# Kernel tuning notes

Hardware: AMD Instinct MI355X
Metric: run time of the kernel (lower is better)

The kernel has to match this reference:

```python
import jax, jax.numpy as jnp
import numpy as np

N_PER_GRAPH = 468
B = 32
N = B * N_PER_GRAPH            # 14976 nodes
E = 89600                      # synthetic Delaunay-like directed edges
IN_DIM, HID, OUT, HEADS = 2, 256, 512, 4
NEG_SLOPE = 0.2
EPS = 1e-16


def setup_inputs() -> dict:
    key = jax.random.key(0)
    ks = jax.random.split(key, 12)
    x = jax.random.uniform(ks[0], (N, IN_DIM), dtype=jnp.float32)
    edge_index = jax.random.randint(ks[1], (2, E), 0, N, dtype=jnp.int64)
    batch = jnp.repeat(jnp.arange(B, dtype=jnp.int64), N_PER_GRAPH)
    s1 = 1.0 / np.sqrt(IN_DIM)
    s2 = 1.0 / np.sqrt(HID)
    sg = 1.0 / np.sqrt(OUT)
    return {
        "x": x,
        "edge_index": edge_index,
        "batch": batch,
        # GATConv 1: in_dim -> hidden, heads=4, concat=False
        "W1": jax.random.normal(ks[2], (IN_DIM, HEADS * HID), jnp.float32) * s1,
        "a1_src": jax.random.normal(ks[3], (HEADS, HID), jnp.float32) * s2,
        "a1_dst": jax.random.normal(ks[4], (HEADS, HID), jnp.float32) * s2,
        "b1": jnp.zeros((HID,), jnp.float32),
        # GATConv 2: hidden -> out, heads=4, concat=False
        "W2": jax.random.normal(ks[5], (HID, HEADS * OUT), jnp.float32) * s2,
        "a2_src": jax.random.normal(ks[6], (HEADS, OUT), jnp.float32) * sg,
        "a2_dst": jax.random.normal(ks[7], (HEADS, OUT), jnp.float32) * sg,
        "b2": jnp.zeros((OUT,), jnp.float32),
        # GlobalAttention gate_nn: Linear(out_dim, 1)
        "Wg": jax.random.normal(ks[8], (OUT, 1), jnp.float32) * sg,
        "bg": jnp.zeros((1,), jnp.float32),
    }


def _gat_layer(x, src, dst, W, a_src, a_dst, b, heads, out_ch):
    n = x.shape[0]
    xh = (x @ W).reshape(n, heads, out_ch)            # [N,H,C]
    alpha_s = jnp.einsum("nhc,hc->nh", xh, a_src)     # [N,H]
    alpha_d = jnp.einsum("nhc,hc->nh", xh, a_dst)
    e = alpha_s[src] + alpha_d[dst]                   # [E,H]
    e = jnp.where(e > 0, e, NEG_SLOPE * e)            # leaky_relu(0.2)
    # segment softmax over incoming edges of each destination node
    m = jax.ops.segment_max(e, dst, num_segments=n)
    ex = jnp.exp(e - m[dst])
    denom = jax.ops.segment_sum(ex, dst, num_segments=n)
    alpha = ex / (denom[dst] + EPS)                   # [E,H]
    msg = xh[src] * alpha[:, :, None]                 # [E,H,C]
    out = jax.ops.segment_sum(msg, dst, num_segments=n)  # [N,H,C]
    return out.mean(axis=1) + b                       # concat=False -> head mean


def reference(x, edge_index, batch, W1, a1_src, a1_dst, b1,
              W2, a2_src, a2_dst, b2, Wg, bg):
    n = x.shape[0]
    # PyG GATConv default add_self_loops=True (both layers use the same graph)
    loops = jnp.arange(n, dtype=edge_index.dtype)
    src = jnp.concatenate([edge_index[0], loops])
    dst = jnp.concatenate([edge_index[1], loops])

    h = _gat_layer(x, src, dst, W1, a1_src, a1_dst, b1, HEADS, HID)
    h = jax.nn.relu(h)
    h = _gat_layer(h, src, dst, W2, a2_src, a2_dst, b2, HEADS, OUT)
    h = jax.nn.relu(h)

    # GlobalAttention pooling: gate = Linear(out,1), softmax per graph, weighted sum
    gate = h @ Wg + bg                                # [N,1]
    gm = jax.ops.segment_max(gate, batch, num_segments=B)
    ge = jnp.exp(gate - gm[batch])
    gs = jax.ops.segment_sum(ge, batch, num_segments=B)
    attn = ge / (gs[batch] + EPS)                     # [N,1]
    pooled = jax.ops.segment_sum(attn * h, batch, num_segments=B)  # [B,512]
    return pooled.reshape(-1, 1, OUT)                 # [B,1,512]
```

## Files before the change

### kernel.cpp

```cpp
#include <hip/hip_runtime.h>
#include <hip/hip_bf16.h>
#include <math.h>

#define HEADS 4
#define C1 256
#define C2 512
#define NEG 0.2f
#define EPSF 1e-16f
#define DCAP 64

using bf16x8 = __attribute__((ext_vector_type(8))) short;
using f32x4  = __attribute__((ext_vector_type(4))) float;

__device__ __forceinline__ float lrelu(float e) { return e > 0.f ? e : NEG * e; }

__device__ __forceinline__ unsigned short f2bf(float v) {
    __hip_bfloat16 b = __float2bfloat16(v);
    return *reinterpret_cast<unsigned short*>(&b);
}
__device__ __forceinline__ float bf2f(unsigned short u) {
    __hip_bfloat16 b = *reinterpret_cast<__hip_bfloat16*>(&u);
    return __bfloat162float(b);
}


__global__ __launch_bounds__(256) void k1_prep(
    const float* __restrict__ x, const float* __restrict__ W1,
    const float* __restrict__ a1s, const float* __restrict__ a1d,
    const float* __restrict__ W2, const float* __restrict__ a2s, const float* __restrict__ a2d,
    const int* __restrict__ ei, int E, int N,
    float* __restrict__ as1, float* __restrict__ ad1,
    float* __restrict__ w2a,
    unsigned short* __restrict__ W2t_hi, unsigned short* __restrict__ W2t_lo,
    int* __restrict__ deg, int* __restrict__ bucket)
{
    int b = blockIdx.x, tid = threadIdx.x;
    int wv = tid >> 6, lane = tid & 63;
    if (b < 59) {
        __shared__ float s_w1a[16];
#pragma unroll
        for (int q = 0; q < 4; q++) {
            int o = wv * 4 + q, sd = o >> 3, idx = o & 7, h = idx >> 1, d = idx & 1;
            const float* av = sd ? a1d : a1s;
            float p = 0.f;
            for (int c = lane; c < 256; c += 64) p += W1[d * 1024 + h * 256 + c] * av[h * 256 + c];
#pragma unroll
            for (int m = 32; m >= 1; m >>= 1) p += __shfl_xor(p, m, 64);
            if (lane == 0) s_w1a[o] = p;
        }
        __syncthreads();
        int n = b * 256 + tid;
        if (n < N) {
            float x0 = x[2 * n], x1 = x[2 * n + 1];
            float4 av, dv;
            float* ap = &av.x; float* dp = &dv.x;
#pragma unroll
            for (int h = 0; h < 4; h++) {
                ap[h] = x0 * s_w1a[h * 2] + x1 * s_w1a[h * 2 + 1];
                dp[h] = x0 * s_w1a[8 + h * 2] + x1 * s_w1a[8 + h * 2 + 1];
            }
            *reinterpret_cast<float4*>(&as1[n * 4]) = av;
            *reinterpret_cast<float4*>(&ad1[n * 4]) = dv;
        }
    } else if (b < 67) {
        int bb = b - 59, sd = bb >> 2, h = bb & 3;
        const float* av = sd ? a2d : a2s;
        float gv[8];
#pragma unroll
        for (int q = 0; q < 8; q++) gv[q] = av[h * 512 + lane * 8 + q];
        for (int k = wv; k < 256; k += 4) {
            const float4 w0 = *reinterpret_cast<const float4*>(&W2[(size_t)k * 2048 + h * 512 + lane * 8]);
            const float4 w1 = *reinterpret_cast<const float4*>(&W2[(size_t)k * 2048 + h * 512 + lane * 8 + 4]);
            float p = w0.x*gv[0] + w0.y*gv[1] + w0.z*gv[2] + w0.w*gv[3]
                    + w1.x*gv[4] + w1.y*gv[5] + w1.z*gv[6] + w1.w*gv[7];
#pragma unroll
            for (int m = 32; m >= 1; m >>= 1) p += __shfl_xor(p, m, 64);
            if (lane == 0) w2a[sd * 1024 + h * 256 + k] = p;
        }
    } else if (b < 195) {
        __shared__ float T[64][65];
        int lin = b - 67;
        int kk0 = (lin & 15) * 64, n0 = (lin >> 4) * 64;
        int h = kk0 >> 8, k0 = kk0 & 255;
#pragma unroll
        for (int rr = 0; rr < 16; rr++) {
            int ki = rr * 4 + (tid >> 6), ni = tid & 63;
            T[ki][ni] = W2[(size_t)(k0 + ki) * 2048 + h * 512 + n0 + ni];
        }
        __syncthreads();
#pragma unroll
        for (int rr = 0; rr < 16; rr++) {
            int ni = rr * 4 + (tid >> 6), ki = tid & 63;
            float v = T[ki][ni];
            unsigned short hi = f2bf(v);
            unsigned short lo = f2bf(v - bf2f(hi));
            size_t o = (size_t)(n0 + ni) * 1024 + kk0 + ki;
            W2t_hi[o] = hi; W2t_lo[o] = lo;
        }
    } else {
        int i = (b - 195) * 256 + tid;
        if (i < E) {
            int s = ei[i], d = ei[E + i];
            int slot = atomicAdd(&deg[d], 1);
            if (slot < DCAP) bucket[d * DCAP + slot] = s;
        }
    }
}

__global__ __launch_bounds__(256) void k4_agg1_h1(
    const float* __restrict__ x, const float* __restrict__ as1, const float* __restrict__ ad1,
    const int* __restrict__ deg, const int* __restrict__ bucket,
    const float* __restrict__ W1, const float* __restrict__ b1, const float* __restrict__ w2a,
    float* __restrict__ h1, float* __restrict__ as2, float* __restrict__ ad2)
{
    int wv = threadIdx.x >> 6, lane = threadIdx.x & 63;
    int n = blockIdx.x * 4 + wv;
    const float4 sa4 = *reinterpret_cast<const float4*>(&as1[n * 4]);
    const float4 da4 = *reinterpret_cast<const float4*>(&ad1[n * 4]);
    const float sa[4] = {sa4.x, sa4.y, sa4.z, sa4.w};
    const float da[4] = {da4.x, da4.y, da4.z, da4.w};
    float acc[8] = {0,0,0,0,0,0,0,0};
    float den[4] = {0,0,0,0};
    int dg = min(deg[n], DCAP);
    for (int i = lane; i < dg; i += 64) {
        int s = bucket[n * DCAP + i];
        const float4 a4 = *reinterpret_cast<const float4*>(&as1[s * 4]);
        const float af[4] = {a4.x, a4.y, a4.z, a4.w};
        const float2 xv = reinterpret_cast<const float2*>(x)[s];
#pragma unroll
        for (int q = 0; q < 4; q++) {
            float w = expf(lrelu(af[q] + da[q]));
            den[q] += w;
            acc[2 * q]     = fmaf(w, xv.x, acc[2 * q]);
            acc[2 * q + 1] = fmaf(w, xv.y, acc[2 * q + 1]);
        }
    }
#pragma unroll
    for (int msk = 1; msk <= 32; msk <<= 1) {
#pragma unroll
        for (int q = 0; q < 8; q++) acc[q] += __shfl_xor(acc[q], msk, 64);
#pragma unroll
        for (int q = 0; q < 4; q++) den[q] += __shfl_xor(den[q], msk, 64);
    }
    const float2 xn = reinterpret_cast<const float2*>(x)[n];
    float xa[8];
#pragma unroll
    for (int q = 0; q < 4; q++) {
        float ws = expf(lrelu(sa[q] + da[q]));
        float dq = den[q] + ws;
        float inv = 1.f / (dq + EPSF);
        xa[2 * q]     = (acc[2 * q]     + ws * xn.x) * inv;
        xa[2 * q + 1] = (acc[2 * q + 1] + ws * xn.y) * inv;
    }
    float t[4] = {0.f, 0.f, 0.f, 0.f};
#pragma unroll
    for (int h = 0; h < 4; h++)
#pragma unroll
        for (int d = 0; d < 2; d++) {
            const float4 w4 = *reinterpret_cast<const float4*>(&W1[d * 1024 + h * 256 + lane * 4]);
            float xx = xa[h * 2 + d];
            t[0] = fmaf(xx, w4.x, t[0]);
            t[1] = fmaf(xx, w4.y, t[1]);
            t[2] = fmaf(xx, w4.z, t[2]);
            t[3] = fmaf(xx, w4.w, t[3]);
        }
    const float4 b4 = *reinterpret_cast<const float4*>(&b1[lane * 4]);
    float v[4];
    v[0] = fmaxf(fmaf(0.25f, t[0], b4.x), 0.f);
    v[1] = fmaxf(fmaf(0.25f, t[1], b4.y), 0.f);
    v[2] = fmaxf(fmaf(0.25f, t[2], b4.z), 0.f);
    v[3] = fmaxf(fmaf(0.25f, t[3], b4.w), 0.f);
    *reinterpret_cast<float4*>(&h1[(size_t)n * 256 + lane * 4]) = make_float4(v[0], v[1], v[2], v[3]);
    float p[8];
#pragma unroll
    for (int o = 0; o < 8; o++) {
        int sd = o >> 2, h = o & 3;
        const float4 w4 = *reinterpret_cast<const float4*>(&w2a[sd * 1024 + h * 256 + lane * 4]);
        p[o] = v[0] * w4.x + v[1] * w4.y + v[2] * w4.z + v[3] * w4.w;
    }
#pragma unroll
    for (int msk = 1; msk <= 32; msk <<= 1)
#pragma unroll
        for (int o = 0; o < 8; o++) p[o] += __shfl_xor(p[o], msk, 64);
    if (lane == 0) {
        *reinterpret_cast<float4*>(&as2[n * 4]) = make_float4(p[0], p[1], p[2], p[3]);
        *reinterpret_cast<float4*>(&ad2[n * 4]) = make_float4(p[4], p[5], p[6], p[7]);
    }
}

__global__ __launch_bounds__(256) void k6_agg2(
    const float* __restrict__ h1, const float* __restrict__ as2, const float* __restrict__ ad2,
    const int* __restrict__ deg, const int* __restrict__ bucket,
    unsigned short* __restrict__ hagg_hi, unsigned short* __restrict__ hagg_lo)
{
    int wv = threadIdx.x >> 6, lane = threadIdx.x & 63;
    int n = blockIdx.x * 4 + wv;
    const float4 sa4 = *reinterpret_cast<const float4*>(&as2[n * 4]);
    const float4 da4 = *reinterpret_cast<const float4*>(&ad2[n * 4]);
    const float sa[4] = {sa4.x, sa4.y, sa4.z, sa4.w};
    const float da[4] = {da4.x, da4.y, da4.z, da4.w};
    float den[4], acc[4][4];
    const float4 hs = *reinterpret_cast<const float4*>(&h1[(size_t)n * 256 + lane * 4]);
    const float hv0[4] = {hs.x, hs.y, hs.z, hs.w};
#pragma unroll
    for (int h = 0; h < 4; h++) {
        float ws = expf(lrelu(sa[h] + da[h]));
        den[h] = ws;
#pragma unroll
        for (int q = 0; q < 4; q++) acc[h][q] = ws * hv0[q];
    }
    int dg = min(deg[n], DCAP);
    for (int i = 0; i < dg; i++) {
        int s = bucket[n * DCAP + i];
        const float4 a4 = *reinterpret_cast<const float4*>(&as2[s * 4]);
        const float af[4] = {a4.x, a4.y, a4.z, a4.w};
        const float4 hv = *reinterpret_cast<const float4*>(&h1[(size_t)s * 256 + lane * 4]);
#pragma unroll
        for (int h = 0; h < 4; h++) {
            float w = expf(lrelu(af[h] + da[h]));
            den[h] += w;
            acc[h][0] = fmaf(w, hv.x, acc[h][0]);
            acc[h][1] = fmaf(w, hv.y, acc[h][1]);
            acc[h][2] = fmaf(w, hv.z, acc[h][2]);
            acc[h][3] = fmaf(w, hv.w, acc[h][3]);
        }
    }
#pragma unroll
    for (int h = 0; h < 4; h++) {
        float inv = 1.f / (den[h] + EPSF);
        ushort4 hi4, lo4;
        unsigned short* hp = &hi4.x; unsigned short* lp = &lo4.x;
#pragma unroll
        for (int q = 0; q < 4; q++) {
            float val = acc[h][q] * inv;
            unsigned short hi = f2bf(val);
            hp[q] = hi;
            lp[q] = f2bf(val - bf2f(hi));
        }
        size_t o = (size_t)n * 1024 + h * 256 + lane * 4;
        *reinterpret_cast<ushort4*>(&hagg_hi[o]) = hi4;
        *reinterpret_cast<ushort4*>(&hagg_lo[o]) = lo4;
    }
}

__global__ __launch_bounds__(256) void k7_gemm2(
    const unsigned short* __restrict__ Ahi, const unsigned short* __restrict__ Alo,
    const unsigned short* __restrict__ Bhi, const unsigned short* __restrict__ Blo,
    const float* __restrict__ b2, const float* __restrict__ Wg,
    float* __restrict__ h2, float* __restrict__ gate)
{
    __shared__ __align__(16) unsigned short As_hi[128 * 40], As_lo[128 * 40];
    __shared__ __align__(16) unsigned short Bs_hi[128 * 40], Bs_lo[128 * 40];
    __shared__ float s_gate[128];
    int tid = threadIdx.x, l = tid & 63, wv = tid >> 6;
    int wr = wv >> 1, wc = wv & 1;
    int bid = blockIdx.x, rtile, ctile;
    if (bid < 448) { rtile = (bid & 7) + 8 * (bid >> 5); ctile = (bid >> 3) & 3; }
    else           { int t = bid - 448; rtile = 112 + (t >> 2); ctile = t & 3; }
    int row0 = rtile * 128, col0 = ctile * 128;
    int lm = l & 15, lg = l >> 4;
    if (tid < 128) s_gate[tid] = 0.f;

    int r0 = tid >> 2, k00 = (tid & 3) * 8;
    int r1 = (tid + 256) >> 2, k01 = ((tid + 256) & 3) * 8;

    f32x4 acc[4][4];
#pragma unroll
    for (int i = 0; i < 4; i++)
#pragma unroll
        for (int jj = 0; jj < 4; jj++) { acc[i][jj][0]=0.f; acc[i][jj][1]=0.f; acc[i][jj][2]=0.f; acc[i][jj][3]=0.f; }

    uint4 pah0, pal0, pbh0, pbl0, pah1, pal1, pbh1, pbl1;
    {
        size_t ga0 = (size_t)(row0 + r0) * 1024 + k00, gb0 = (size_t)(col0 + r0) * 1024 + k00;
        size_t ga1 = (size_t)(row0 + r1) * 1024 + k01, gb1 = (size_t)(col0 + r1) * 1024 + k01;
        pah0 = *reinterpret_cast<const uint4*>(Ahi + ga0); pal0 = *reinterpret_cast<const uint4*>(Alo + ga0);
        pbh0 = *reinterpret_cast<const uint4*>(Bhi + gb0); pbl0 = *reinterpret_cast<const uint4*>(Blo + gb0);
        pah1 = *reinterpret_cast<const uint4*>(Ahi + ga1); pal1 = *reinterpret_cast<const uint4*>(Alo + ga1);
        pbh1 = *reinterpret_cast<const uint4*>(Bhi + gb1); pbl1 = *reinterpret_cast<const uint4*>(Blo + gb1);
    }

    for (int kt = 0; kt < 1024; kt += 32) {
        *reinterpret_cast<uint4*>(&As_hi[r0 * 40 + k00]) = pah0;
        *reinterpret_cast<uint4*>(&As_lo[r0 * 40 + k00]) = pal0;
        *reinterpret_cast<uint4*>(&Bs_hi[r0 * 40 + k00]) = pbh0;
        *reinterpret_cast<uint4*>(&Bs_lo[r0 * 40 + k00]) = pbl0;
        *reinterpret_cast<uint4*>(&As_hi[r1 * 40 + k01]) = pah1;
        *reinterpret_cast<uint4*>(&As_lo[r1 * 40 + k01]) = pal1;
        *reinterpret_cast<uint4*>(&Bs_hi[r1 * 40 + k01]) = pbh1;
        *reinterpret_cast<uint4*>(&Bs_lo[r1 * 40 + k01]) = pbl1;
        __syncthreads();
        if (kt + 32 < 1024) {
            int ktn = kt + 32;
            size_t ga0 = (size_t)(row0 + r0) * 1024 + ktn + k00, gb0 = (size_t)(col0 + r0) * 1024 + ktn + k00;
            size_t ga1 = (size_t)(row0 + r1) * 1024 + ktn + k01, gb1 = (size_t)(col0 + r1) * 1024 + ktn + k01;
            pah0 = *reinterpret_cast<const uint4*>(Ahi + ga0); pal0 = *reinterpret_cast<const uint4*>(Alo + ga0);
            pbh0 = *reinterpret_cast<const uint4*>(Bhi + gb0); pbl0 = *reinterpret_cast<const uint4*>(Blo + gb0);
            pah1 = *reinterpret_cast<const uint4*>(Ahi + ga1); pal1 = *reinterpret_cast<const uint4*>(Alo + ga1);
            pbh1 = *reinterpret_cast<const uint4*>(Bhi + gb1); pbl1 = *reinterpret_cast<const uint4*>(Blo + gb1);
        }
        bf16x8 ah[4], al[4], bh[4], bl[4];
#pragma unroll
        for (int i = 0; i < 4; i++) {
            int base = (wr * 64 + i * 16 + lm) * 40 + lg * 8;
            ah[i] = *reinterpret_cast<const bf16x8*>(&As_hi[base]);
            al[i] = *reinterpret_cast<const bf16x8*>(&As_lo[base]);
        }
#pragma unroll
        for (int jj = 0; jj < 4; jj++) {
            int base = (wc * 64 + jj * 16 + lm) * 40 + lg * 8;
            bh[jj] = *reinterpret_cast<const bf16x8*>(&Bs_hi[base]);
            bl[jj] = *reinterpret_cast<const bf16x8*>(&Bs_lo[base]);
        }
#pragma unroll
        for (int i = 0; i < 4; i++)
#pragma unroll
            for (int jj = 0; jj < 4; jj++) {
                acc[i][jj] = __builtin_amdgcn_mfma_f32_16x16x32_bf16(ah[i], bh[jj], acc[i][jj], 0, 0, 0);
                acc[i][jj] = __builtin_amdgcn_mfma_f32_16x16x32_bf16(ah[i], bl[jj], acc[i][jj], 0, 0, 0);
                acc[i][jj] = __builtin_amdgcn_mfma_f32_16x16x32_bf16(al[i], bh[jj], acc[i][jj], 0, 0, 0);
            }
        __syncthreads();
    }
    float b2c[4], wgj[4];
#pragma unroll
    for (int jj = 0; jj < 4; jj++) {
        int col = col0 + wc * 64 + jj * 16 + lm;
        b2c[jj] = b2[col]; wgj[jj] = Wg[col];
    }
#pragma unroll
    for (int i = 0; i < 4; i++) {
#pragma unroll
        for (int r = 0; r < 4; r++) {
            int row = row0 + wr * 64 + i * 16 + lg * 4 + r;
            float g = 0.f;
#pragma unroll
            for (int jj = 0; jj < 4; jj++) {
                float v = fmaxf(fmaf(0.25f, acc[i][jj][r], b2c[jj]), 0.f);
                h2[(size_t)row * 512 + col0 + wc * 64 + jj * 16 + lm] = v;
                g = fmaf(v, wgj[jj], g);
            }
            g += __shfl_xor(g, 1, 64);
            g += __shfl_xor(g, 2, 64);
            g += __shfl_xor(g, 4, 64);
            g += __shfl_xor(g, 8, 64);
            if (lm == 0) atomicAdd(&s_gate[wr * 64 + i * 16 + lg * 4 + r], g);
        }
    }
    __syncthreads();
    if (tid < 128) atomicAdd(&gate[row0 + tid], s_gate[tid]);
}

__global__ __launch_bounds__(256) void k8_pool(
    const float* __restrict__ gate, const float* __restrict__ h2,
    float* __restrict__ out, int npg)
{
    int bq = blockIdx.x, cs = blockIdx.y, tid = threadIdx.x;
    int n0 = bq * npg;
    __shared__ float sw[512];
    __shared__ float sred[4];
    __shared__ float4 sacc[256];
    float part = 0.f;
    for (int i = tid; i < 512; i += 256) {
        float e = (i < npg) ? expf(gate[n0 + i]) : 0.f;
        sw[i] = e; part += e;
    }
#pragma unroll
    for (int m = 32; m >= 1; m >>= 1) part += __shfl_xor(part, m, 64);
    if ((tid & 63) == 0) sred[tid >> 6] = part;
    __syncthreads();
    float inv = 1.f / (sred[0] + sred[1] + sred[2] + sred[3] + EPSF);
    int slot = tid & 31, sub = tid >> 5;
    const float* base = h2 + (size_t)n0 * 512 + cs * 128 + slot * 4;
    float4 acc = make_float4(0.f, 0.f, 0.f, 0.f);
    for (int i = sub; i < npg; i += 8) {
        float w = sw[i];
        const float4 v = *reinterpret_cast<const float4*>(base + (size_t)i * 512);
        acc.x = fmaf(w, v.x, acc.x);
        acc.y = fmaf(w, v.y, acc.y);
        acc.z = fmaf(w, v.z, acc.z);
        acc.w = fmaf(w, v.w, acc.w);
    }
    sacc[tid] = acc;
    __syncthreads();
    if (sub == 0) {
        float4 t = acc;
#pragma unroll
        for (int s2 = 1; s2 < 8; s2++) {
            const float4 o = sacc[s2 * 32 + slot];
            t.x += o.x; t.y += o.y; t.z += o.z; t.w += o.w;
        }
        t.x *= inv; t.y *= inv; t.z *= inv; t.w *= inv;
        *reinterpret_cast<float4*>(&out[(size_t)bq * 512 + cs * 128 + slot * 4]) = t;
    }
}

extern "C" void kernel_launch(void* const* d_in, const int* in_sizes, int n_in,
                              void* d_out, int out_size, void* d_ws, size_t ws_size,
                              hipStream_t stream)
{
    const float* x    = (const float*)d_in[0];
    const int*   ei   = (const int*)d_in[1];
    const float* W1   = (const float*)d_in[3];
    const float* a1s  = (const float*)d_in[4];
    const float* a1d  = (const float*)d_in[5];
    const float* b1   = (const float*)d_in[6];
    const float* W2   = (const float*)d_in[7];
    const float* a2s  = (const float*)d_in[8];
    const float* a2d  = (const float*)d_in[9];
    const float* b2   = (const float*)d_in[10];
    const float* Wg   = (const float*)d_in[11];
    float* out = (float*)d_out;

    const int N = in_sizes[0] / 2;
    const int E = in_sizes[1] / 2;
    const int Bq = out_size / C2;
    const int npg = N / Bq;

    char* w = (char*)d_ws;
    size_t off = 0;
    auto alloc = [&](size_t bytes) { void* p = w + off; off += (bytes + 255) & ~(size_t)255; return p; };

    float* h1       = (float*)alloc((size_t)N * 256 * 4);
    float* h2       = (float*)alloc((size_t)N * 512 * 4);
    unsigned short* hagg_hi = (unsigned short*)alloc((size_t)N * 1024 * 2);
    unsigned short* hagg_lo = (unsigned short*)alloc((size_t)N * 1024 * 2);
    unsigned short* W2t_hi  = (unsigned short*)alloc((size_t)512 * 1024 * 2);
    unsigned short* W2t_lo  = (unsigned short*)alloc((size_t)512 * 1024 * 2);
    float* as1   = (float*)alloc((size_t)N * 4 * 4);
    float* ad1   = (float*)alloc((size_t)N * 4 * 4);
    float* as2   = (float*)alloc((size_t)N * 4 * 4);
    float* ad2   = (float*)alloc((size_t)N * 4 * 4);
    int*   deg   = (int*)alloc((size_t)N * 4);
    float* gate  = (float*)alloc((size_t)N * 4);
    float* w2a   = (float*)alloc(2048 * 4);
    int*   bucket = (int*)alloc((size_t)N * DCAP * 4);
    (void)ws_size; (void)n_in;

    const int EB = (E + 255) / 256;

    hipMemsetAsync(deg, 0, (size_t)N * 4 * 2, stream);

    k1_prep<<<195 + EB, 256, 0, stream>>>(x, W1, a1s, a1d, W2, a2s, a2d, ei, E, N,
                                          as1, ad1, w2a, W2t_hi, W2t_lo, deg, bucket);
    k4_agg1_h1<<<N / 4, 256, 0, stream>>>(x, as1, ad1, deg, bucket,
                                          W1, b1, w2a, h1, as2, ad2);
    k6_agg2<<<N / 4, 256, 0, stream>>>(h1, as2, ad2, deg, bucket, hagg_hi, hagg_lo);
    k7_gemm2<<<468, 256, 0, stream>>>(hagg_hi, hagg_lo, W2t_hi, W2t_lo,
                                      b2, Wg, h2, gate);
    k8_pool<<<dim3(Bq, 4), 256, 0, stream>>>(gate, h2, out, npg);
}
```

Baseline: 251.4 us.

## Fuse pipeline into two persistent kernels with software grid barriers

Merges prep, layer-1 aggregation and layer-2 aggregation into one persistent kernel, and the GEMM plus pooling into a second, separated by atomic-counter grid barriers. This removes kernel launch gaps and boundaries between stages. The pooling stage is also split across more blocks. It relies on all blocks being co-resident, and the barriers add spin cost; grid-stride loops over the aggregation replace one-block-per-4-nodes launches.

```diff
diff --git a/kernel.cpp b/kernel.cpp
--- a/kernel.cpp
+++ b/kernel.cpp
@@ -23,235 +23,258 @@
     return __bfloat162float(b);
 }
 
-
-__global__ __launch_bounds__(256) void k1_prep(
+__device__ __forceinline__ void gbar(int* cnt, int* gen, int nb, int e) {
+    __syncthreads();
+    if (threadIdx.x == 0) {
+        __threadfence();
+        int v = __hip_atomic_fetch_add(cnt, 1, __ATOMIC_RELAXED, __HIP_MEMORY_SCOPE_AGENT);
+        if (v == nb * e - 1) {
+            __hip_atomic_fetch_add(gen, 1, __ATOMIC_RELEASE, __HIP_MEMORY_SCOPE_AGENT);
+        } else {
+            while (__hip_atomic_load(gen, __ATOMIC_RELAXED, __HIP_MEMORY_SCOPE_AGENT) < e)
+                __builtin_amdgcn_s_sleep(2);
+        }
+        __threadfence();
+    }
+    __syncthreads();
+}
+
+
+#define M1_GRID 1024
+__global__ __launch_bounds__(256, 4) void mega1(
     const float* __restrict__ x, const float* __restrict__ W1,
     const float* __restrict__ a1s, const float* __restrict__ a1d,
     const float* __restrict__ W2, const float* __restrict__ a2s, const float* __restrict__ a2d,
     const int* __restrict__ ei, int E, int N,
+    const float* __restrict__ b1,
     float* __restrict__ as1, float* __restrict__ ad1,
     float* __restrict__ w2a,
     unsigned short* __restrict__ W2t_hi, unsigned short* __restrict__ W2t_lo,
-    int* __restrict__ deg, int* __restrict__ bucket)
+    int* __restrict__ deg, int* __restrict__ bucket,
+    float* __restrict__ h1, float* __restrict__ as2, float* __restrict__ ad2,
+    unsigned short* __restrict__ hagg_hi, unsigned short* __restrict__ hagg_lo,
+    int* __restrict__ bcnt, int* __restrict__ bgen)
 {
-    int b = blockIdx.x, tid = threadIdx.x;
+    __shared__ float T[64][65];
+    __shared__ float s_w1a[16];
+    int bid = blockIdx.x, tid = threadIdx.x;
     int wv = tid >> 6, lane = tid & 63;
-    if (b < 59) {
-        __shared__ float s_w1a[16];
+
+    {
+        int b = bid;
+        if (b < 59) {
+#pragma unroll
+            for (int q = 0; q < 4; q++) {
+                int o = wv * 4 + q, sd = o >> 3, idx = o & 7, h = idx >> 1, d = idx & 1;
+                const float* av = sd ? a1d : a1s;
+                float p = 0.f;
+                for (int c = lane; c < 256; c += 64) p += W1[d * 1024 + h * 256 + c] * av[h * 256 + c];
+#pragma unroll
+                for (int m = 32; m >= 1; m >>= 1) p += __shfl_xor(p, m, 64);
+                if (lane == 0) s_w1a[o] = p;
+            }
+            __syncthreads();
+            int n = b * 256 + tid;
+            if (n < N) {
+                float x0 = x[2 * n], x1 = x[2 * n + 1];
+                float4 av, dv;
+                float* ap = &av.x; float* dp = &dv.x;
+#pragma unroll
+                for (int h = 0; h < 4; h++) {
+                    ap[h] = x0 * s_w1a[h * 2] + x1 * s_w1a[h * 2 + 1];
+                    dp[h] = x0 * s_w1a[8 + h * 2] + x1 * s_w1a[8 + h * 2 + 1];
+                }
+                *reinterpret_cast<float4*>(&as1[n * 4]) = av;
+                *reinterpret_cast<float4*>(&ad1[n * 4]) = dv;
+            }
+        } else if (b < 67) {
+            int bb = b - 59, sd = bb >> 2, h = bb & 3;
+            const float* av = sd ? a2d : a2s;
+            float gv[8];
+#pragma unroll
+            for (int q = 0; q < 8; q++) gv[q] = av[h * 512 + lane * 8 + q];
+            for (int k = wv; k < 256; k += 4) {
+                const float4 w0 = *reinterpret_cast<const float4*>(&W2[(size_t)k * 2048 + h * 512 + lane * 8]);
+                const float4 w1 = *reinterpret_cast<const float4*>(&W2[(size_t)k * 2048 + h * 512 + lane * 8 + 4]);
+                float p = w0.x*gv[0] + w0.y*gv[1] + w0.z*gv[2] + w0.w*gv[3]
+                        + w1.x*gv[4] + w1.y*gv[5] + w1.z*gv[6] + w1.w*gv[7];
+#pragma unroll
+                for (int m = 32; m >= 1; m >>= 1) p += __shfl_xor(p, m, 64);
+                if (lane == 0) w2a[sd * 1024 + h * 256 + k] = p;
+            }
+        } else if (b < 195) {
+            int lin = b - 67;
+            int kk0 = (lin & 15) * 64, n0 = (lin >> 4) * 64;
+            int h = kk0 >> 8, k0 = kk0 & 255;
+#pragma unroll
+            for (int rr = 0; rr < 16; rr++) {
+                int ki = rr * 4 + (tid >> 6), ni = tid & 63;
+                T[ki][ni] = W2[(size_t)(k0 + ki) * 2048 + h * 512 + n0 + ni];
+            }
+            __syncthreads();
+#pragma unroll
+            for (int rr = 0; rr < 16; rr++) {
+                int ni = rr * 4 + (tid >> 6), ki = tid & 63;
+                float v = T[ki][ni];
+                unsigned short hi = f2bf(v);
+                unsigned short lo = f2bf(v - bf2f(hi));
+                size_t o = (size_t)(n0 + ni) * 1024 + kk0 + ki;
+                W2t_hi[o] = hi; W2t_lo[o] = lo;
+            }
+        } else if (b < 545) {
+            int i = (b - 195) * 256 + tid;
+            if (i < E) {
+                int s = ei[i], d = ei[E + i];
+                int slot = atomicAdd(&deg[d], 1);
+                if (slot < DCAP) bucket[d * DCAP + slot] = s;
+            }
+        }
+    }
+    gbar(bcnt, bgen, M1_GRID, 1);
+
+    for (int vb = bid; vb < N / 4; vb += M1_GRID) {
+        int n = vb * 4 + wv;
+        const float4 sa4 = *reinterpret_cast<const float4*>(&as1[n * 4]);
+        const float4 da4 = *reinterpret_cast<const float4*>(&ad1[n * 4]);
+        const float sa[4] = {sa4.x, sa4.y, sa4.z, sa4.w};
+        const float da[4] = {da4.x, da4.y, da4.z, da4.w};
+        float acc[8] = {0,0,0,0,0,0,0,0};
+        float den[4] = {0,0,0,0};
+        int dg = min(deg[n], DCAP);
+        for (int i = lane; i < dg; i += 64) {
+            int s = bucket[n * DCAP + i];
+            const float4 a4 = *reinterpret_cast<const float4*>(&as1[s * 4]);
+            const float af[4] = {a4.x, a4.y, a4.z, a4.w};
+            const float2 xv = reinterpret_cast<const float2*>(x)[s];
+#pragma unroll
+            for (int q = 0; q < 4; q++) {
+                float w = expf(lrelu(af[q] + da[q]));
+                den[q] += w;
+                acc[2 * q]     = fmaf(w, xv.x, acc[2 * q]);
+                acc[2 * q + 1] = fmaf(w, xv.y, acc[2 * q + 1]);
+            }
+        }
+#pragma unroll
+        for (int msk = 1; msk <= 32; msk <<= 1) {
+#pragma unroll
+            for (int q = 0; q < 8; q++) acc[q] += __shfl_xor(acc[q], msk, 64);
+#pragma unroll
+            for (int q = 0; q < 4; q++) den[q] += __shfl_xor(den[q], msk, 64);
+        }
+        const float2 xn = reinterpret_cast<const float2*>(x)[n];
+        float xa[8];
 #pragma unroll
         for (int q = 0; q < 4; q++) {
-            int o = wv * 4 + q, sd = o >> 3, idx = o & 7, h = idx >> 1, d = idx & 1;
-            const float* av = sd ? a1d : a1s;
-            float p = 0.f;
-            for (int c = lane; c < 256; c += 64) p += W1[d * 1024 + h * 256 + c] * av[h * 256 + c];
-#pragma unroll
-            for (int m = 32; m >= 1; m >>= 1) p += __shfl_xor(p, m, 64);
-            if (lane == 0) s_w1a[o] = p;
-        }
-        __syncthreads();
-        int n = b * 256 + tid;
-        if (n < N) {
-            float x0 = x[2 * n], x1 = x[2 * n + 1];
-            float4 av, dv;
-            float* ap = &av.x; float* dp = &dv.x;
+            float ws = expf(lrelu(sa[q] + da[q]));
+            float dq = den[q] + ws;
+            float inv = 1.f / (dq + EPSF);
+            xa[2 * q]     = (acc[2 * q]     + ws * xn.x) * inv;
+            xa[2 * q + 1] = (acc[2 * q + 1] + ws * xn.y) * inv;
+        }
+        float t[4] = {0.f, 0.f, 0.f, 0.f};
+#pragma unroll
+        for (int h = 0; h < 4; h++)
+#pragma unroll
+            for (int d = 0; d < 2; d++) {
+                const float4 w4 = *reinterpret_cast<const float4*>(&W1[d * 1024 + h * 256 + lane * 4]);
+                float xx = xa[h * 2 + d];
+                t[0] = fmaf(xx, w4.x, t[0]);
+                t[1] = fmaf(xx, w4.y, t[1]);
+                t[2] = fmaf(xx, w4.z, t[2]);
+                t[3] = fmaf(xx, w4.w, t[3]);
+            }
+        const float4 b4 = *reinterpret_cast<const float4*>(&b1[lane * 4]);
+        float v[4];
+        v[0] = fmaxf(fmaf(0.25f, t[0], b4.x), 0.f);
+        v[1] = fmaxf(fmaf(0.25f, t[1], b4.y), 0.f);
+        v[2] = fmaxf(fmaf(0.25f, t[2], b4.z), 0.f);
+        v[3] = fmaxf(fmaf(0.25f, t[3], b4.w), 0.f);
+        *reinterpret_cast<float4*>(&h1[(size_t)n * 256 + lane * 4]) = make_float4(v[0], v[1], v[2], v[3]);
+        float p[8];
+#pragma unroll
+        for (int o = 0; o < 8; o++) {
+            int sd = o >> 2, h = o & 3;
+            const float4 w4 = *reinterpret_cast<const float4*>(&w2a[sd * 1024 + h * 256 + lane * 4]);
+            p[o] = v[0] * w4.x + v[1] * w4.y + v[2] * w4.z + v[3] * w4.w;
+        }
+#pragma unroll
+        for (int msk = 1; msk <= 32; msk <<= 1)
+#pragma unroll
+            for (int o = 0; o < 8; o++) p[o] += __shfl_xor(p[o], msk, 64);
+        if (lane == 0) {
+            *reinterpret_cast<float4*>(&as2[n * 4]) = make_float4(p[0], p[1], p[2], p[3]);
+            *reinterpret_cast<float4*>(&ad2[n * 4]) = make_float4(p[4], p[5], p[6], p[7]);
+        }
+    }
+    gbar(bcnt, bgen, M1_GRID, 2);
+
+    for (int vb = bid; vb < N / 4; vb += M1_GRID) {
+        int n = vb * 4 + wv;
+        const float4 sa4 = *reinterpret_cast<const float4*>(&as2[n * 4]);
+        const float4 da4 = *reinterpret_cast<const float4*>(&ad2[n * 4]);
+        const float sa[4] = {sa4.x, sa4.y, sa4.z, sa4.w};
+        const float da[4] = {da4.x, da4.y, da4.z, da4.w};
+        float den[4], acc[4][4];
+        const float4 hs = *reinterpret_cast<const float4*>(&h1[(size_t)n * 256 + lane * 4]);
+        const float hv0[4] = {hs.x, hs.y, hs.z, hs.w};
+#pragma unroll
+        for (int h = 0; h < 4; h++) {
+            float ws = expf(lrelu(sa[h] + da[h]));
+            den[h] = ws;
+#pragma unroll
+            for (int q = 0; q < 4; q++) acc[h][q] = ws * hv0[q];
+        }
+        int dg = min(deg[n], DCAP);
+        for (int i = 0; i < dg; i++) {
+            int s = bucket[n * DCAP + i];
+            const float4 a4 = *reinterpret_cast<const float4*>(&as2[s * 4]);
+            const float af[4] = {a4.x, a4.y, a4.z, a4.w};
+            const float4 hv = *reinterpret_cast<const float4*>(&h1[(size_t)s * 256 + lane * 4]);
 #pragma unroll
             for (int h = 0; h < 4; h++) {
-                ap[h] = x0 * s_w1a[h * 2] + x1 * s_w1a[h * 2 + 1];
-                dp[h] = x0 * s_w1a[8 + h * 2] + x1 * s_w1a[8 + h * 2 + 1];
-            }
-            *reinterpret_cast<float4*>(&as1[n * 4]) = av;
-            *reinterpret_cast<float4*>(&ad1[n * 4]) = dv;
-        }
-    } else if (b < 67) {
-        int bb = b - 59, sd = bb >> 2, h = bb & 3;
-        const float* av = sd ? a2d : a2s;
-        float gv[8];
-#pragma unroll
-        for (int q = 0; q < 8; q++) gv[q] = av[h * 512 + lane * 8 + q];
-        for (int k = wv; k < 256; k += 4) {
-            const float4 w0 = *reinterpret_cast<const float4*>(&W2[(size_t)k * 2048 + h * 512 + lane * 8]);
-            const float4 w1 = *reinterpret_cast<const float4*>(&W2[(size_t)k * 2048 + h * 512 + lane * 8 + 4]);
-            float p = w0.x*gv[0] + w0.y*gv[1] + w0.z*gv[2] + w0.w*gv[3]
-                    + w1.x*gv[4] + w1.y*gv[5] + w1.z*gv[6] + w1.w*gv[7];
-#pragma unroll
-            for (int m = 32; m >= 1; m >>= 1) p += __shfl_xor(p, m, 64);
-            if (lane == 0) w2a[sd * 1024 + h * 256 + k] = p;
-        }
-    } else if (b < 195) {
-        __shared__ float T[64][65];
-        int lin = b - 67;
-        int kk0 = (lin & 15) * 64, n0 = (lin >> 4) * 64;
-        int h = kk0 >> 8, k0 = kk0 & 255;
-#pragma unroll
-        for (int rr = 0; rr < 16; rr++) {
-            int ki = rr * 4 + (tid >> 6), ni = tid & 63;
-            T[ki][ni] = W2[(size_t)(k0 + ki) * 2048 + h * 512 + n0 + ni];
-        }
-        __syncthreads();
-#pragma unroll
-        for (int rr = 0; rr < 16; rr++) {
-            int ni = rr * 4 + (tid >> 6), ki = tid & 63;
-            float v = T[ki][ni];
-            unsigned short hi = f2bf(v);
-            unsigned short lo = f2bf(v - bf2f(hi));
-            size_t o = (size_t)(n0 + ni) * 1024 + kk0 + ki;
-            W2t_hi[o] = hi; W2t_lo[o] = lo;
-        }
-    } else {
-        int i = (b - 195) * 256 + tid;
-        if (i < E) {
-            int s = ei[i], d = ei[E + i];
-            int slot = atomicAdd(&deg[d], 1);
-            if (slot < DCAP) bucket[d * DCAP + slot] = s;
-        }
-    }
-}
-
-__global__ __launch_bounds__(256) void k4_agg1_h1(
-    const float* __restrict__ x, const float* __restrict__ as1, const float* __restrict__ ad1,
-    const int* __restrict__ deg, const int* __restrict__ bucket,
-    const float* __restrict__ W1, const float* __restrict__ b1, const float* __restrict__ w2a,
-    float* __restrict__ h1, float* __restrict__ as2, float* __restrict__ ad2)
-{
-    int wv = threadIdx.x >> 6, lane = threadIdx.x & 63;
-    int n = blockIdx.x * 4 + wv;
-    const float4 sa4 = *reinterpret_cast<const float4*>(&as1[n * 4]);
-    const float4 da4 = *reinterpret_cast<const float4*>(&ad1[n * 4]);
-    const float sa[4] = {sa4.x, sa4.y, sa4.z, sa4.w};
-    const float da[4] = {da4.x, da4.y, da4.z, da4.w};
-    float acc[8] = {0,0,0,0,0,0,0,0};
-    float den[4] = {0,0,0,0};
-    int dg = min(deg[n], DCAP);
-    for (int i = lane; i < dg; i += 64) {
-        int s = bucket[n * DCAP + i];
-        const float4 a4 = *reinterpret_cast<const float4*>(&as1[s * 4]);
-        const float af[4] = {a4.x, a4.y, a4.z, a4.w};
-        const float2 xv = reinterpret_cast<const float2*>(x)[s];
-#pragma unroll
-        for (int q = 0; q < 4; q++) {
-            float w = expf(lrelu(af[q] + da[q]));
-            den[q] += w;
-            acc[2 * q]     = fmaf(w, xv.x, acc[2 * q]);
-            acc[2 * q + 1] = fmaf(w, xv.y, acc[2 * q + 1]);
-        }
-    }
-#pragma unroll
-    for (int msk = 1; msk <= 32; msk <<= 1) {
-#pragma unroll
-        for (int q = 0; q < 8; q++) acc[q] += __shfl_xor(acc[q], msk, 64);
-#pragma unroll
-        for (int q = 0; q < 4; q++) den[q] += __shfl_xor(den[q], msk, 64);
-    }
-    const float2 xn = reinterpret_cast<const float2*>(x)[n];
-    float xa[8];
-#pragma unroll
-    for (int q = 0; q < 4; q++) {
-        float ws = expf(lrelu(sa[q] + da[q]));
-        float dq = den[q] + ws;
-        float inv = 1.f / (dq + EPSF);
-        xa[2 * q]     = (acc[2 * q]     + ws * xn.x) * inv;
-        xa[2 * q + 1] = (acc[2 * q + 1] + ws * xn.y) * inv;
-    }
-    float t[4] = {0.f, 0.f, 0.f, 0.f};
-#pragma unroll
-    for (int h = 0; h < 4; h++)
-#pragma unroll
-        for (int d = 0; d < 2; d++) {
-            const float4 w4 = *reinterpret_cast<const float4*>(&W1[d * 1024 + h * 256 + lane * 4]);
-            float xx = xa[h * 2 + d];
-            t[0] = fmaf(xx, w4.x, t[0]);
-            t[1] = fmaf(xx, w4.y, t[1]);
-            t[2] = fmaf(xx, w4.z, t[2]);
-            t[3] = fmaf(xx, w4.w, t[3]);
-        }
-    const float4 b4 = *reinterpret_cast<const float4*>(&b1[lane * 4]);
-    float v[4];
-    v[0] = fmaxf(fmaf(0.25f, t[0], b4.x), 0.f);
-    v[1] = fmaxf(fmaf(0.25f, t[1], b4.y), 0.f);
-    v[2] = fmaxf(fmaf(0.25f, t[2], b4.z), 0.f);
-    v[3] = fmaxf(fmaf(0.25f, t[3], b4.w), 0.f);
-    *reinterpret_cast<float4*>(&h1[(size_t)n * 256 + lane * 4]) = make_float4(v[0], v[1], v[2], v[3]);
-    float p[8];
-#pragma unroll
-    for (int o = 0; o < 8; o++) {
-        int sd = o >> 2, h = o & 3;
-        const float4 w4 = *reinterpret_cast<const float4*>(&w2a[sd * 1024 + h * 256 + lane * 4]);
-        p[o] = v[0] * w4.x + v[1] * w4.y + v[2] * w4.z + v[3] * w4.w;
-    }
-#pragma unroll
-    for (int msk = 1; msk <= 32; msk <<= 1)
-#pragma unroll
-        for (int o = 0; o < 8; o++) p[o] += __shfl_xor(p[o], msk, 64);
-    if (lane == 0) {
-        *reinterpret_cast<float4*>(&as2[n * 4]) = make_float4(p[0], p[1], p[2], p[3]);
-        *reinterpret_cast<float4*>(&ad2[n * 4]) = make_float4(p[4], p[5], p[6], p[7]);
-    }
-}
-
-__global__ __launch_bounds__(256) void k6_agg2(
-    const float* __restrict__ h1, const float* __restrict__ as2, const float* __restrict__ ad2,
-    const int* __restrict__ deg, const int* __restrict__ bucket,
-    unsigned short* __restrict__ hagg_hi, unsigned short* __restrict__ hagg_lo)
-{
-    int wv = threadIdx.x >> 6, lane = threadIdx.x & 63;
-    int n = blockIdx.x * 4 + wv;
-    const float4 sa4 = *reinterpret_cast<const float4*>(&as2[n * 4]);
-    const float4 da4 = *reinterpret_cast<const float4*>(&ad2[n * 4]);
-    const float sa[4] = {sa4.x, sa4.y, sa4.z, sa4.w};
-    const float da[4] = {da4.x, da4.y, da4.z, da4.w};
-    float den[4], acc[4][4];
-    const float4 hs = *reinterpret_cast<const float4*>(&h1[(size_t)n * 256 + lane * 4]);
-    const float hv0[4] = {hs.x, hs.y, hs.z, hs.w};
-#pragma unroll
-    for (int h = 0; h < 4; h++) {
-        float ws = expf(lrelu(sa[h] + da[h]));
-        den[h] = ws;
-#pragma unroll
-        for (int q = 0; q < 4; q++) acc[h][q] = ws * hv0[q];
-    }
-    int dg = min(deg[n], DCAP);
-    for (int i = 0; i < dg; i++) {
-        int s = bucket[n * DCAP + i];
-        const float4 a4 = *reinterpret_cast<const float4*>(&as2[s * 4]);
-        const float af[4] = {a4.x, a4.y, a4.z, a4.w};
-        const float4 hv = *reinterpret_cast<const float4*>(&h1[(size_t)s * 256 + lane * 4]);
+                float w = expf(lrelu(af[h] + da[h]));
+                den[h] += w;
+                acc[h][0] = fmaf(w, hv.x, acc[h][0]);
+                acc[h][1] = fmaf(w, hv.y, acc[h][1]);
+                acc[h][2] = fmaf(w, hv.z, acc[h][2]);
+                acc[h][3] = fmaf(w, hv.w, acc[h][3]);
+            }
+        }
 #pragma unroll
         for (int h = 0; h < 4; h++) {
-            float w = expf(lrelu(af[h] + da[h]));
-            den[h] += w;
-            acc[h][0] = fmaf(w, hv.x, acc[h][0]);
-            acc[h][1] = fmaf(w, hv.y, acc[h][1]);
-            acc[h][2] = fmaf(w, hv.z, acc[h][2]);
-            acc[h][3] = fmaf(w, hv.w, acc[h][3]);
-        }
-    }
-#pragma unroll
-    for (int h = 0; h < 4; h++) {
-        float inv = 1.f / (den[h] + EPSF);
-        ushort4 hi4, lo4;
-        unsigned short* hp = &hi4.x; unsigned short* lp = &lo4.x;
-#pragma unroll
-        for (int q = 0; q < 4; q++) {
-            float val = acc[h][q] * inv;
-            unsigned short hi = f2bf(val);
-            hp[q] = hi;
-            lp[q] = f2bf(val - bf2f(hi));
-        }
-        size_t o = (size_t)n * 1024 + h * 256 + lane * 4;
-        *reinterpret_cast<ushort4*>(&hagg_hi[o]) = hi4;
-        *reinterpret_cast<ushort4*>(&hagg_lo[o]) = lo4;
-    }
-}
-
-__global__ __launch_bounds__(256) void k7_gemm2(
+            float inv = 1.f / (den[h] + EPSF);
+            ushort4 hi4, lo4;
+            unsigned short* hp = &hi4.x; unsigned short* lp = &lo4.x;
+#pragma unroll
+            for (int q = 0; q < 4; q++) {
+                float val = acc[h][q] * inv;
+                unsigned short hi = f2bf(val);
+                hp[q] = hi;
+                lp[q] = f2bf(val - bf2f(hi));
+            }
+            size_t o = (size_t)n * 1024 + h * 256 + lane * 4;
+            *reinterpret_cast<ushort4*>(&hagg_hi[o]) = hi4;
+            *reinterpret_cast<ushort4*>(&hagg_lo[o]) = lo4;
+        }
+    }
+}
+
+#define M2_GRID 468
+__global__ __launch_bounds__(256, 3) void mega2(
     const unsigned short* __restrict__ Ahi, const unsigned short* __restrict__ Alo,
     const unsigned short* __restrict__ Bhi, const unsigned short* __restrict__ Blo,
     const float* __restrict__ b2, const float* __restrict__ Wg,
-    float* __restrict__ h2, float* __restrict__ gate)
+    float* __restrict__ h2, float* __restrict__ gate,
+    float* __restrict__ out, int npg,
+    int* __restrict__ bcnt, int* __restrict__ bgen)
 {
-    __shared__ __align__(16) unsigned short As_hi[128 * 40], As_lo[128 * 40];
-    __shared__ __align__(16) unsigned short Bs_hi[128 * 40], Bs_lo[128 * 40];
-    __shared__ float s_gate[128];
+    __shared__ __align__(16) char smem[41472];
+    unsigned short* As_hi = (unsigned short*)(smem);
+    unsigned short* As_lo = (unsigned short*)(smem + 10240);
+    unsigned short* Bs_hi = (unsigned short*)(smem + 20480);
+    unsigned short* Bs_lo = (unsigned short*)(smem + 30720);
+    float* s_gate = (float*)(smem + 40960);
+
     int tid = threadIdx.x, l = tid & 63, wv = tid >> 6;
     int wr = wv >> 1, wc = wv & 1;
     int bid = blockIdx.x, rtile, ctile;
@@ -349,49 +372,48 @@
     }
     __syncthreads();
     if (tid < 128) atomicAdd(&gate[row0 + tid], s_gate[tid]);
-}
-
-__global__ __launch_bounds__(256) void k8_pool(
-    const float* __restrict__ gate, const float* __restrict__ h2,
-    float* __restrict__ out, int npg)
-{
-    int bq = blockIdx.x, cs = blockIdx.y, tid = threadIdx.x;
-    int n0 = bq * npg;
-    __shared__ float sw[512];
-    __shared__ float sred[4];
-    __shared__ float4 sacc[256];
-    float part = 0.f;
-    for (int i = tid; i < 512; i += 256) {
-        float e = (i < npg) ? expf(gate[n0 + i]) : 0.f;
-        sw[i] = e; part += e;
-    }
-#pragma unroll
-    for (int m = 32; m >= 1; m >>= 1) part += __shfl_xor(part, m, 64);
-    if ((tid & 63) == 0) sred[tid >> 6] = part;
-    __syncthreads();
-    float inv = 1.f / (sred[0] + sred[1] + sred[2] + sred[3] + EPSF);
-    int slot = tid & 31, sub = tid >> 5;
-    const float* base = h2 + (size_t)n0 * 512 + cs * 128 + slot * 4;
-    float4 acc = make_float4(0.f, 0.f, 0.f, 0.f);
-    for (int i = sub; i < npg; i += 8) {
-        float w = sw[i];
-        const float4 v = *reinterpret_cast<const float4*>(base + (size_t)i * 512);
-        acc.x = fmaf(w, v.x, acc.x);
-        acc.y = fmaf(w, v.y, acc.y);
-        acc.z = fmaf(w, v.z, acc.z);
-        acc.w = fmaf(w, v.w, acc.w);
-    }
-    sacc[tid] = acc;
-    __syncthreads();
-    if (sub == 0) {
-        float4 t = acc;
-#pragma unroll
-        for (int s2 = 1; s2 < 8; s2++) {
-            const float4 o = sacc[s2 * 32 + slot];
-            t.x += o.x; t.y += o.y; t.z += o.z; t.w += o.w;
-        }
-        t.x *= inv; t.y *= inv; t.z *= inv; t.w *= inv;
-        *reinterpret_cast<float4*>(&out[(size_t)bq * 512 + cs * 128 + slot * 4]) = t;
+
+    gbar(bcnt, bgen, M2_GRID, 1);
+
+    if (bid < 256) {
+        float* sw   = (float*)(smem);
+        float* sred = (float*)(smem + 2048);
+        float4* sacc = (float4*)(smem + 2176);
+        int bq = bid >> 3, cs = bid & 7;
+        int n0 = bq * npg;
+        float part = 0.f;
+        for (int i = tid; i < 512; i += 256) {
+            float e = (i < npg) ? expf(gate[n0 + i]) : 0.f;
+            sw[i] = e; part += e;
+        }
+#pragma unroll
+        for (int m = 32; m >= 1; m >>= 1) part += __shfl_xor(part, m, 64);
+        if ((tid & 63) == 0) sred[tid >> 6] = part;
+        __syncthreads();
+        float inv = 1.f / (sred[0] + sred[1] + sred[2] + sred[3] + EPSF);
+        int slot = tid & 15, sub = tid >> 4;
+        const float* base = h2 + (size_t)n0 * 512 + cs * 64 + slot * 4;
+        float4 acc2 = make_float4(0.f, 0.f, 0.f, 0.f);
+        for (int i = sub; i < npg; i += 16) {
+            float w = sw[i];
+            const float4 v = *reinterpret_cast<const float4*>(base + (size_t)i * 512);
+            acc2.x = fmaf(w, v.x, acc2.x);
+            acc2.y = fmaf(w, v.y, acc2.y);
+            acc2.z = fmaf(w, v.z, acc2.z);
+            acc2.w = fmaf(w, v.w, acc2.w);
+        }
+        sacc[tid] = acc2;
+        __syncthreads();
+        if (sub == 0) {
+            float4 t = acc2;
+#pragma unroll
+            for (int s2 = 1; s2 < 16; s2++) {
+                const float4 o = sacc[s2 * 16 + slot];
+                t.x += o.x; t.y += o.y; t.z += o.z; t.w += o.w;
+            }
+            t.x *= inv; t.y *= inv; t.z *= inv; t.w *= inv;
+            *reinterpret_cast<float4*>(&out[(size_t)bq * 512 + cs * 64 + slot * 4]) = t;
+        }
     }
 }
 
@@ -433,20 +455,17 @@
     float* ad2   = (float*)alloc((size_t)N * 4 * 4);
     int*   deg   = (int*)alloc((size_t)N * 4);
     float* gate  = (float*)alloc((size_t)N * 4);
+    int*   bars  = (int*)alloc(256);
     float* w2a   = (float*)alloc(2048 * 4);
     int*   bucket = (int*)alloc((size_t)N * DCAP * 4);
     (void)ws_size; (void)n_in;
 
-    const int EB = (E + 255) / 256;
-
-    hipMemsetAsync(deg, 0, (size_t)N * 4 * 2, stream);
-
-    k1_prep<<<195 + EB, 256, 0, stream>>>(x, W1, a1s, a1d, W2, a2s, a2d, ei, E, N,
-                                          as1, ad1, w2a, W2t_hi, W2t_lo, deg, bucket);
-    k4_agg1_h1<<<N / 4, 256, 0, stream>>>(x, as1, ad1, deg, bucket,
-                                          W1, b1, w2a, h1, as2, ad2);
-    k6_agg2<<<N / 4, 256, 0, stream>>>(h1, as2, ad2, deg, bucket, hagg_hi, hagg_lo);
-    k7_gemm2<<<468, 256, 0, stream>>>(hagg_hi, hagg_lo, W2t_hi, W2t_lo,
-                                      b2, Wg, h2, gate);
-    k8_pool<<<dim3(Bq, 4), 256, 0, stream>>>(gate, h2, out, npg);
-}
+    hipMemsetAsync(deg, 0, (size_t)N * 8 + 256, stream);
+
+    mega1<<<M1_GRID, 256, 0, stream>>>(x, W1, a1s, a1d, W2, a2s, a2d, ei, E, N, b1,
+                                       as1, ad1, w2a, W2t_hi, W2t_lo, deg, bucket,
+                                       h1, as2, ad2, hagg_hi, hagg_lo,
+                                       &bars[0], &bars[1]);
+    mega2<<<M2_GRID, 256, 0, stream>>>(hagg_hi, hagg_lo, W2t_hi, W2t_lo, b2, Wg,
+                                       h2, gate, out, npg, &bars[2], &bars[3]);
+}
```

Measured after the change: 503.3 us. 100% more time.

## Pre-swizzle GEMM operands into MFMA fragment layout and drop LDS staging

Applied to the files above, without the earlier changes.

The aggregation kernel and the weight-prep kernel now write the bf16 hi/lo operands directly in per-16-row, per-32-K MFMA fragment order. The GEMM kernel then loads each lane's bf16x8 fragments straight from global memory with register double buffering, so the shared-memory tiles and per-iteration barriers are gone. The aim is to remove LDS traffic and synchronisation from the GEMM. In exchange, each wave now loads its fragments separately with no sharing across waves in a block, which raises global/L2 traffic and register pressure.

```diff
diff --git a/kernel.cpp b/kernel.cpp
--- a/kernel.cpp
+++ b/kernel.cpp
@@ -94,7 +94,10 @@
             float v = T[ki][ni];
             unsigned short hi = f2bf(v);
             unsigned short lo = f2bf(v - bf2f(hi));
-            size_t o = (size_t)(n0 + ni) * 1024 + kk0 + ki;
+            int rowp = n0 + ni, kg = kk0 + ki;
+            int kt = kg >> 5, cb = rowp >> 4;
+            int ll = (rowp & 15) | (((kg >> 3) & 3) << 4);
+            size_t o = ((size_t)(kt * 32 + cb) * 64 + ll) * 8 + (kg & 7);
             W2t_hi[o] = hi; W2t_lo[o] = lo;
         }
     } else {
@@ -191,7 +194,7 @@
 __global__ __launch_bounds__(256) void k6_agg2(
     const float* __restrict__ h1, const float* __restrict__ as2, const float* __restrict__ ad2,
     const int* __restrict__ deg, const int* __restrict__ bucket,
-    unsigned short* __restrict__ hagg_hi, unsigned short* __restrict__ hagg_lo)
+    unsigned short* __restrict__ hagg_hi, unsigned short* __restrict__ hagg_lo, int nrb)
 {
     int wv = threadIdx.x >> 6, lane = threadIdx.x & 63;
     int n = blockIdx.x * 4 + wv;
@@ -225,6 +228,9 @@
             acc[h][3] = fmaf(w, hv.w, acc[h][3]);
         }
     }
+    int rb = n >> 4;
+    int ll = (n & 15) | (((lane >> 1) & 3) << 4);
+    int jj0 = (lane & 1) * 4;
 #pragma unroll
     for (int h = 0; h < 4; h++) {
         float inv = 1.f / (den[h] + EPSF);
@@ -237,20 +243,30 @@
             hp[q] = hi;
             lp[q] = f2bf(val - bf2f(hi));
         }
-        size_t o = (size_t)n * 1024 + h * 256 + lane * 4;
+        int kt = h * 8 + (lane >> 3);
+        size_t o = ((size_t)(kt * nrb + rb) * 64 + ll) * 8 + jj0;
         *reinterpret_cast<ushort4*>(&hagg_hi[o]) = hi4;
         *reinterpret_cast<ushort4*>(&hagg_lo[o]) = lo4;
     }
 }
+
+#define K7_PREF(S, KT) do { int _ao = aoff + (KT) * astep, _bo = boff + (KT) * 2048; \
+    _Pragma("unroll") for (int i = 0; i < 4; i++) { \
+        S##ah[i] = pAh[_ao + i * 64]; S##al[i] = pAl[_ao + i * 64]; \
+        S##bh[i] = pBh[_bo + i * 64]; S##bl[i] = pBl[_bo + i * 64]; } } while (0)
+
+#define K7_MFMA(S) do { _Pragma("unroll") for (int i = 0; i < 4; i++) \
+    _Pragma("unroll") for (int jj = 0; jj < 4; jj++) { \
+        acc[i][jj] = __builtin_amdgcn_mfma_f32_16x16x32_bf16(S##ah[i], S##bh[jj], acc[i][jj], 0, 0, 0); \
+        acc[i][jj] = __builtin_amdgcn_mfma_f32_16x16x32_bf16(S##ah[i], S##bl[jj], acc[i][jj], 0, 0, 0); \
+        acc[i][jj] = __builtin_amdgcn_mfma_f32_16x16x32_bf16(S##al[i], S##bh[jj], acc[i][jj], 0, 0, 0); } } while (0)
 
 __global__ __launch_bounds__(256) void k7_gemm2(
     const unsigned short* __restrict__ Ahi, const unsigned short* __restrict__ Alo,
     const unsigned short* __restrict__ Bhi, const unsigned short* __restrict__ Blo,
     const float* __restrict__ b2, const float* __restrict__ Wg,
-    float* __restrict__ h2, float* __restrict__ gate)
-{
-    __shared__ __align__(16) unsigned short As_hi[128 * 40], As_lo[128 * 40];
-    __shared__ __align__(16) unsigned short Bs_hi[128 * 40], Bs_lo[128 * 40];
+    float* __restrict__ h2, float* __restrict__ gate, int nrb)
+{
     __shared__ float s_gate[128];
     int tid = threadIdx.x, l = tid & 63, wv = tid >> 6;
     int wr = wv >> 1, wc = wv & 1;
@@ -261,8 +277,13 @@
     int lm = l & 15, lg = l >> 4;
     if (tid < 128) s_gate[tid] = 0.f;
 
-    int r0 = tid >> 2, k00 = (tid & 3) * 8;
-    int r1 = (tid + 256) >> 2, k01 = ((tid + 256) & 3) * 8;
+    const bf16x8* pAh = (const bf16x8*)Ahi;
+    const bf16x8* pAl = (const bf16x8*)Alo;
+    const bf16x8* pBh = (const bf16x8*)Bhi;
+    const bf16x8* pBl = (const bf16x8*)Blo;
+    int aoff = (rtile * 8 + wr * 4) * 64 + l;
+    int boff = (ctile * 8 + wc * 4) * 64 + l;
+    const int astep = nrb * 64;
 
     f32x4 acc[4][4];
 #pragma unroll
@@ -270,58 +291,17 @@
 #pragma unroll
         for (int jj = 0; jj < 4; jj++) { acc[i][jj][0]=0.f; acc[i][jj][1]=0.f; acc[i][jj][2]=0.f; acc[i][jj][3]=0.f; }
 
-    uint4 pah0, pal0, pbh0, pbl0, pah1, pal1, pbh1, pbl1;
-    {
-        size_t ga0 = (size_t)(row0 + r0) * 1024 + k00, gb0 = (size_t)(col0 + r0) * 1024 + k00;
-        size_t ga1 = (size_t)(row0 + r1) * 1024 + k01, gb1 = (size_t)(col0 + r1) * 1024 + k01;
-        pah0 = *reinterpret_cast<const uint4*>(Ahi + ga0); pal0 = *reinterpret_cast<const uint4*>(Alo + ga0);
-        pbh0 = *reinterpret_cast<const uint4*>(Bhi + gb0); pbl0 = *reinterpret_cast<const uint4*>(Blo + gb0);
-        pah1 = *reinterpret_cast<const uint4*>(Ahi + ga1); pal1 = *reinterpret_cast<const uint4*>(Alo + ga1);
-        pbh1 = *reinterpret_cast<const uint4*>(Bhi + gb1); pbl1 = *reinterpret_cast<const uint4*>(Blo + gb1);
-    }
-
-    for (int kt = 0; kt < 1024; kt += 32) {
-        *reinterpret_cast<uint4*>(&As_hi[r0 * 40 + k00]) = pah0;
-        *reinterpret_cast<uint4*>(&As_lo[r0 * 40 + k00]) = pal0;
-        *reinterpret_cast<uint4*>(&Bs_hi[r0 * 40 + k00]) = pbh0;
-        *reinterpret_cast<uint4*>(&Bs_lo[r0 * 40 + k00]) = pbl0;
-        *reinterpret_cast<uint4*>(&As_hi[r1 * 40 + k01]) = pah1;
-        *reinterpret_cast<uint4*>(&As_lo[r1 * 40 + k01]) = pal1;
-        *reinterpret_cast<uint4*>(&Bs_hi[r1 * 40 + k01]) = pbh1;
-        *reinterpret_cast<uint4*>(&Bs_lo[r1 * 40 + k01]) = pbl1;
-        __syncthreads();
-        if (kt + 32 < 1024) {
-            int ktn = kt + 32;
-            size_t ga0 = (size_t)(row0 + r0) * 1024 + ktn + k00, gb0 = (size_t)(col0 + r0) * 1024 + ktn + k00;
-            size_t ga1 = (size_t)(row0 + r1) * 1024 + ktn + k01, gb1 = (size_t)(col0 + r1) * 1024 + ktn + k01;
-            pah0 = *reinterpret_cast<const uint4*>(Ahi + ga0); pal0 = *reinterpret_cast<const uint4*>(Alo + ga0);
-            pbh0 = *reinterpret_cast<const uint4*>(Bhi + gb0); pbl0 = *reinterpret_cast<const uint4*>(Blo + gb0);
-            pah1 = *reinterpret_cast<const uint4*>(Ahi + ga1); pal1 = *reinterpret_cast<const uint4*>(Alo + ga1);
-            pbh1 = *reinterpret_cast<const uint4*>(Bhi + gb1); pbl1 = *reinterpret_cast<const uint4*>(Blo + gb1);
-        }
-        bf16x8 ah[4], al[4], bh[4], bl[4];
-#pragma unroll
-        for (int i = 0; i < 4; i++) {
-            int base = (wr * 64 + i * 16 + lm) * 40 + lg * 8;
-            ah[i] = *reinterpret_cast<const bf16x8*>(&As_hi[base]);
-            al[i] = *reinterpret_cast<const bf16x8*>(&As_lo[base]);
-        }
-#pragma unroll
-        for (int jj = 0; jj < 4; jj++) {
-            int base = (wc * 64 + jj * 16 + lm) * 40 + lg * 8;
-            bh[jj] = *reinterpret_cast<const bf16x8*>(&Bs_hi[base]);
-            bl[jj] = *reinterpret_cast<const bf16x8*>(&Bs_lo[base]);
-        }
-#pragma unroll
-        for (int i = 0; i < 4; i++)
-#pragma unroll
-            for (int jj = 0; jj < 4; jj++) {
-                acc[i][jj] = __builtin_amdgcn_mfma_f32_16x16x32_bf16(ah[i], bh[jj], acc[i][jj], 0, 0, 0);
-                acc[i][jj] = __builtin_amdgcn_mfma_f32_16x16x32_bf16(ah[i], bl[jj], acc[i][jj], 0, 0, 0);
-                acc[i][jj] = __builtin_amdgcn_mfma_f32_16x16x32_bf16(al[i], bh[jj], acc[i][jj], 0, 0, 0);
-            }
-        __syncthreads();
-    }
+    bf16x8 pah[4], pal[4], pbh[4], pbl[4];
+    bf16x8 qah[4], qal[4], qbh[4], qbl[4];
+    K7_PREF(p, 0);
+    for (int kt = 0; kt < 32; kt += 2) {
+        K7_PREF(q, kt + 1);
+        K7_MFMA(p);
+        if (kt + 2 < 32) K7_PREF(p, kt + 2);
+        K7_MFMA(q);
+    }
+    __syncthreads();
+
     float b2c[4], wgj[4];
 #pragma unroll
     for (int jj = 0; jj < 4; jj++) {
@@ -416,6 +396,7 @@
     const int E = in_sizes[1] / 2;
     const int Bq = out_size / C2;
     const int npg = N / Bq;
+    const int nrb = N >> 4;
 
     char* w = (char*)d_ws;
     size_t off = 0;
@@ -445,8 +426,8 @@
                                           as1, ad1, w2a, W2t_hi, W2t_lo, deg, bucket);
     k4_agg1_h1<<<N / 4, 256, 0, stream>>>(x, as1, ad1, deg, bucket,
                                           W1, b1, w2a, h1, as2, ad2);
-    k6_agg2<<<N / 4, 256, 0, stream>>>(h1, as2, ad2, deg, bucket, hagg_hi, hagg_lo);
+    k6_agg2<<<N / 4, 256, 0, stream>>>(h1, as2, ad2, deg, bucket, hagg_hi, hagg_lo, nrb);
     k7_gemm2<<<468, 256, 0, stream>>>(hagg_hi, hagg_lo, W2t_hi, W2t_lo,
-                                      b2, Wg, h2, gate);
+                                      b2, Wg, h2, gate, nrb);
     k8_pool<<<dim3(Bq, 4), 256, 0, stream>>>(gate, h2, out, npg);
 }
```

New measurement: 264.0 us. 5.0% more time.
